# Performance work log

Measured on AMD Instinct MI355X. Metric: run time of the kernel, lower is better.

Reference implementation:

```python
import jax, jax.numpy as jnp
import numpy as np

EPS = 1e-3  # keras BatchNormalization default epsilon


def _bn(x, gamma, beta, mean, var):
    # inference-mode batch norm over last axis
    return gamma * (x - mean) * jax.lax.rsqrt(var + EPS) + beta


def _maxpool_w2(x):
    # MaxPooling2D(pool_size=[1,2], strides=[1,2]) over width axis of NHWC
    B, H, W, C = x.shape
    return x.reshape(B, H, W // 2, 2, C).max(axis=3)


def setup_inputs() -> dict:
    key = jax.random.key(0)
    ks = jax.random.split(key, 12)
    B, H, W, C, Ci = 8, 64, 64, 256, 128
    s = lambda k, shape, scale=0.05: jax.random.normal(k, shape, dtype=jnp.float32) * scale
    return {
        "inputs": jax.random.normal(ks[0], (B, H, W, C), dtype=jnp.float32),
        "bn1_gamma": jnp.ones((C,), jnp.float32), "bn1_beta": jnp.zeros((C,), jnp.float32),
        "bn1_mean": s(ks[1], (C,), 0.1), "bn1_var": jnp.abs(s(ks[2], (C,), 0.1)) + 1.0,
        "bn2_gamma": jnp.ones((Ci,), jnp.float32), "bn2_beta": jnp.zeros((Ci,), jnp.float32),
        "bn2_mean": s(ks[3], (Ci,), 0.1), "bn2_var": jnp.abs(s(ks[4], (Ci,), 0.1)) + 1.0,
        "W_g": s(ks[5], (C, Ci)), "b_g": jnp.zeros((Ci,), jnp.float32),
        "W_theta": s(ks[6], (C, Ci)), "b_theta": jnp.zeros((Ci,), jnp.float32),
        "W_phi": s(ks[7], (C, Ci)), "b_phi": jnp.zeros((Ci,), jnp.float32),
        "W_z": s(ks[8], (Ci, C)), "b_z": jnp.zeros((C,), jnp.float32),
        "sita": s(ks[9], (1,), 0.5),
    }


def reference(inputs, bn1_gamma, bn1_beta, bn1_mean, bn1_var,
              bn2_gamma, bn2_beta, bn2_mean, bn2_var,
              W_g, b_g, W_theta, b_theta, W_phi, b_phi, W_z, b_z, sita):
    B, H, W, C = inputs.shape
    Ci = W_g.shape[1]
    x = jax.nn.elu(_bn(inputs, bn1_gamma, bn1_beta, bn1_mean, bn1_var))
    # 1x1 convs == per-pixel channel matmuls (NHWC)
    g_x = _maxpool_w2(jnp.einsum('bhwc,cd->bhwd', x, W_g) + b_g)          # [B,H,W/2,Ci]
    g_x = g_x.reshape(B, H * (W // 2), Ci)                                  # [B,Ns,Ci]
    theta_x = (jnp.einsum('bhwc,cd->bhwd', x, W_theta) + b_theta).reshape(B, H * W, Ci)  # [B,N,Ci]
    phi_x = _maxpool_w2(jnp.einsum('bhwc,cd->bhwd', x, W_phi) + b_phi)    # [B,H,W/2,Ci]
    phi_x = phi_x.transpose(0, 3, 1, 2).reshape(B, Ci, H * (W // 2))        # [B,Ci,Ns]
    f = jnp.einsum('bnc,bcm->bnm', theta_x, phi_x)                          # [B,N,Ns]
    y = jax.nn.softmax(f, axis=-1)
    y = jnp.einsum('bnm,bmc->bnc', y, g_x).reshape(B, H, W, Ci)
    fre_z = jax.nn.elu(_bn(y, bn2_gamma, bn2_beta, bn2_mean, bn2_var))
    fre_z = jnp.einsum('bhwc,cd->bhwd', fre_z, W_z) + b_z                   # [B,H,W,C]
    return fre_z * sita + inputs
```

## Files before the change

kernel.cpp:

```cpp
#include <hip/hip_runtime.h>
#include <math.h>

#define BNEPS 1e-3f
#define LOG2E 1.44269504f

typedef __attribute__((ext_vector_type(8))) short bf8;
typedef __attribute__((ext_vector_type(8))) unsigned short u16x8;
typedef __attribute__((ext_vector_type(16))) float f32x16;
typedef __attribute__((ext_vector_type(2))) unsigned u32x2;

__device__ __forceinline__ unsigned short f2bf(float x) {
  unsigned u = __builtin_bit_cast(unsigned, x);
  unsigned r = (u + 0x7fffu + ((u >> 16) & 1u)) >> 16;
  return (unsigned short)r;
}
__device__ __forceinline__ float bf2f(unsigned short h) {
  return __builtin_bit_cast(float, ((unsigned)h) << 16);
}
__device__ __forceinline__ float eluf(float v) { return v > 0.f ? v : expm1f(v); }
__device__ __forceinline__ unsigned cvtpk(float a, float b) {
  unsigned r;
  asm("v_cvt_pk_bf16_f32 %0, %1, %2" : "=v"(r) : "v"(a), "v"(b));
  return r;
}
__device__ __forceinline__ float exp2a(float x) {
  float r;
  asm("v_exp_f32 %0, %1" : "=v"(r) : "v"(x));
  return r;
}

#define GLDS(src, dst)                                                          \
  __builtin_amdgcn_global_load_lds(                                             \
      (const __attribute__((address_space(1))) unsigned int*)(src),             \
      (__attribute__((address_space(3))) unsigned int*)(dst), 16, 0, 0)

__global__ __launch_bounds__(256) void k_prepw(
    const float* __restrict__ Wth, const float* __restrict__ Wg,
    const float* __restrict__ Wph, const float* __restrict__ Wz,
    const float* __restrict__ g1, const float* __restrict__ b1,
    const float* __restrict__ m1, const float* __restrict__ v1,
    const float* __restrict__ g2, const float* __restrict__ b2,
    const float* __restrict__ m2, const float* __restrict__ v2,
    unsigned short* __restrict__ Wt3, unsigned short* __restrict__ Wzt,
    float* __restrict__ bn1s, float* __restrict__ bn1h,
    float* __restrict__ bn2s, float* __restrict__ bn2h)
{
  int id = blockIdx.x * 256 + threadIdx.x;
  if (id < 98304) {
    int w = id >> 15, rem = id & 32767;
    int n = rem >> 8, k = rem & 255;
    const float* W = (w == 0) ? Wth : (w == 1) ? Wg : Wph;
    Wt3[id] = f2bf(W[(size_t)k * 128 + n]);
  } else {
    int rem = id - 98304;
    int n = rem >> 7, k = rem & 127;
    Wzt[rem] = f2bf(Wz[(size_t)k * 256 + n]);
  }
  if (id < 256) { float s = g1[id] * rsqrtf(v1[id] + BNEPS); bn1s[id] = s; bn1h[id] = b1[id] - m1[id] * s; }
  if (id < 128) { float s = g2[id] * rsqrtf(v2[id] + BNEPS); bn2s[id] = s; bn2h[id] = b2[id] - m2[id] * s; }
}

__global__ __launch_bounds__(256) void k_gemm3(
    const float* __restrict__ inp, const float* __restrict__ bn1s,
    const float* __restrict__ bn1h, const unsigned short* __restrict__ Wt3,
    const float* __restrict__ bth, const float* __restrict__ bg,
    const float* __restrict__ bph, unsigned short* __restrict__ Tb,
    unsigned short* __restrict__ Gt2, unsigned short* __restrict__ Pp2)
{
  __shared__ unsigned short As[128][72];
  __shared__ unsigned short Bs[128][72];
  const int bm = blockIdx.x * 128;
  const int sel = blockIdx.y;
  const unsigned short* W = Wt3 + (size_t)sel * 32768;
  const float* bias = (sel == 0) ? bth : (sel == 1) ? bg : bph;
  const int tid = threadIdx.x;
  const int l = tid & 63, w = tid >> 6;
  const int lo = l & 31, g = l >> 5;
  const int row = tid >> 1, hf = tid & 1;
  f32x16 acc[4];
#pragma unroll
  for (int i = 0; i < 4; ++i)
#pragma unroll
    for (int j = 0; j < 16; ++j) acc[i][j] = 0.f;

  for (int k0 = 0; k0 < 256; k0 += 64) {
    __syncthreads();
    {
      const float* sa = inp + (size_t)(bm + row) * 256 + k0 + hf * 32;
      unsigned short tmp[32];
#pragma unroll
      for (int i = 0; i < 8; ++i) {
        float4 v = *(const float4*)(sa + i * 4);
        int ch = k0 + hf * 32 + i * 4;
        tmp[i * 4 + 0] = f2bf(eluf(v.x * bn1s[ch + 0] + bn1h[ch + 0]));
        tmp[i * 4 + 1] = f2bf(eluf(v.y * bn1s[ch + 1] + bn1h[ch + 1]));
        tmp[i * 4 + 2] = f2bf(eluf(v.z * bn1s[ch + 2] + bn1h[ch + 2]));
        tmp[i * 4 + 3] = f2bf(eluf(v.w * bn1s[ch + 3] + bn1h[ch + 3]));
      }
#pragma unroll
      for (int i = 0; i < 4; ++i)
        *(u16x8*)&As[row][hf * 32 + i * 8] = *(u16x8*)&tmp[i * 8];
      const unsigned short* sb = W + (size_t)row * 256 + k0 + hf * 32;
#pragma unroll
      for (int i = 0; i < 4; ++i)
        *(u16x8*)&Bs[row][hf * 32 + i * 8] = *(const u16x8*)(sb + i * 8);
    }
    __syncthreads();
#pragma unroll
    for (int ks = 0; ks < 4; ++ks) {
      bf8 af = *(const bf8*)&As[w * 32 + lo][ks * 16 + g * 8];
#pragma unroll
      for (int n2 = 0; n2 < 4; ++n2) {
        bf8 bF = *(const bf8*)&Bs[n2 * 32 + lo][ks * 16 + g * 8];
        acc[n2] = __builtin_amdgcn_mfma_f32_32x32x16_bf16(af, bF, acc[n2], 0, 0, 0);
      }
    }
  }

  if (sel == 0) {
#pragma unroll
    for (int n2 = 0; n2 < 4; ++n2) {
      int col = n2 * 32 + lo;
      float bv = bias[col];
#pragma unroll
      for (int q = 0; q < 4; ++q)
#pragma unroll
        for (int j = 0; j < 4; ++j) {
          size_t r = (size_t)(bm + w * 32 + j + q * 8 + g * 4);
          Tb[r * 128 + col] = f2bf((acc[n2][q * 4 + j] + bv) * LOG2E);
        }
    }
  } else {
#pragma unroll
    for (int n2 = 0; n2 < 4; ++n2) {
      int col = n2 * 32 + lo;
      float bv = bias[col];
#pragma unroll
      for (int q = 0; q < 4; ++q)
#pragma unroll
        for (int jp = 0; jp < 2; ++jp) {
          int j = jp * 2;
          float v0 = acc[n2][q * 4 + j] + bv;
          float v1 = acc[n2][q * 4 + j + 1] + bv;
          float mx = fmaxf(v0, v1);
          int r = bm + w * 32 + q * 8 + g * 4 + j;
          int pr = r >> 1;
          int b = pr >> 11, local = pr & 2047;
          int kb = local >> 5, sub = (local >> 3) & 3, m = local & 7, kv5 = local & 31;
          if (sel == 1)
            Gt2[((((size_t)b * 64 + kb) * 4 + sub) * 128 + col) * 8 + m] = f2bf(mx);
          else
            Pp2[((((size_t)b * 64 + kb) * 16 + (col >> 3)) * 32 + kv5) * 8 + (col & 7)] = f2bf(mx);
        }
    }
  }
}

__global__ __launch_bounds__(128, 4) void k_attn(
    const unsigned short* __restrict__ T, const unsigned short* __restrict__ Pp2,
    const unsigned short* __restrict__ Gt2, unsigned short* __restrict__ Opart,
    float* __restrict__ lpart)
{
  __shared__ unsigned short phl[4096];
  __shared__ unsigned short vtl[4096];
  const int bid = blockIdx.x;
  const int b = bid & 7, qt = (bid >> 3) & 63, sp = bid >> 9;
  const int tid = threadIdx.x;
  const int w = tid >> 6, l = tid & 63;
  const int lo = l & 31, g = l >> 5;
  const int qr0 = qt * 64;

  const unsigned short* Tq = T + ((size_t)(b * 4096 + qr0 + w * 32 + lo)) * 128 + g * 8;
  bf8 qf[8];
#pragma unroll
  for (int ks = 0; ks < 8; ++ks) qf[ks] = *(const bf8*)(Tq + ks * 16);

  f32x16 oacc[4];
#pragma unroll
  for (int i = 0; i < 4; ++i)
#pragma unroll
    for (int j = 0; j < 16; ++j) oacc[i][j] = 0.f;
  float lrun = 0.f;

  const unsigned short* Pc = Pp2 + ((size_t)b * 64 + sp * 16) * 4096;
  const unsigned short* Gc = Gt2 + ((size_t)b * 64 + sp * 16) * 4096;

  for (int it = 0; it < 16; ++it) {
    const unsigned short* ps = Pc + (size_t)it * 4096 + w * 2048 + l * 8;
    const unsigned short* vs = Gc + (size_t)it * 4096 + w * 2048 + l * 8;
#pragma unroll
    for (int j = 0; j < 4; ++j) {
      GLDS(ps + j * 512, &phl[(w * 4 + j) * 512]);
      GLDS(vs + j * 512, &vtl[(w * 4 + j) * 512]);
    }
    __syncthreads();

    f32x16 s0;
#pragma unroll
    for (int j = 0; j < 16; ++j) s0[j] = 0.f;
#pragma unroll
    for (int ks = 0; ks < 8; ++ks) {
      bf8 a0 = *(const bf8*)&phl[(ks * 2 + g) * 256 + lo * 8];
      s0 = __builtin_amdgcn_mfma_f32_32x32x16_bf16(a0, qf[ks], s0, 0, 0, 0);
    }

#pragma unroll
    for (int r = 0; r < 16; ++r) { s0[r] = exp2a(s0[r]); lrun += s0[r]; }

#pragma unroll
    for (int ks2 = 0; ks2 < 2; ++ks2) {
      const int base = 8 * ks2;
      unsigned uA0 = cvtpk(s0[base + 0], s0[base + 1]);
      unsigned uA1 = cvtpk(s0[base + 2], s0[base + 3]);
      unsigned uB0 = cvtpk(s0[base + 4], s0[base + 5]);
      unsigned uB1 = cvtpk(s0[base + 6], s0[base + 7]);
      unsigned sw0 = g ? uA0 : uB0;
      unsigned sw1 = g ? uA1 : uB1;
      unsigned a0 = sw0, b0 = sw0, a1 = sw1, b1 = sw1;
      asm("v_permlane32_swap_b32 %0, %1" : "+v"(a0), "+v"(b0));
      asm("v_permlane32_swap_b32 %0, %1" : "+v"(a1), "+v"(b1));
      unsigned r0 = g ? a0 : b0;
      unsigned r1 = g ? a1 : b1;
      union { bf8 v; unsigned u[4]; } pf;
      if (g == 0) { pf.u[0] = uA0; pf.u[1] = uA1; pf.u[2] = r0; pf.u[3] = r1; }
      else        { pf.u[0] = r0;  pf.u[1] = r1;  pf.u[2] = uB0; pf.u[3] = uB1; }
#pragma unroll
      for (int n2 = 0; n2 < 4; ++n2) {
        bf8 vf = *(const bf8*)&vtl[(ks2 * 2 + g) * 1024 + (n2 * 32 + lo) * 8];
        oacc[n2] = __builtin_amdgcn_mfma_f32_32x32x16_bf16(vf, pf.v, oacc[n2], 0, 0, 0);
      }
    }
    __syncthreads();
  }

  lrun += __shfl_xor(lrun, 32);
  const int qrow = qr0 + w * 32 + lo;
  unsigned short* Ob = Opart + (size_t)sp * 4194304 + ((size_t)(b * 4096 + qrow)) * 128;
#pragma unroll
  for (int n2 = 0; n2 < 4; ++n2)
#pragma unroll
    for (int q4 = 0; q4 < 4; ++q4) {
      unsigned u0 = cvtpk(oacc[n2][q4 * 4 + 0], oacc[n2][q4 * 4 + 1]);
      unsigned u1 = cvtpk(oacc[n2][q4 * 4 + 2], oacc[n2][q4 * 4 + 3]);
      u32x2 o = {u0, u1};
      *(u32x2*)&Ob[n2 * 32 + q4 * 8 + g * 4] = o;
    }
  if (g == 0) lpart[(size_t)sp * 32768 + b * 4096 + qrow] = lrun;
}

__global__ __launch_bounds__(256) void k_gemm_z(
    const unsigned short* __restrict__ Opart, const float* __restrict__ lp,
    const unsigned short* __restrict__ Wzt,
    const float* __restrict__ bz, const float* __restrict__ bn2s,
    const float* __restrict__ bn2h, const float* __restrict__ inp,
    const float* __restrict__ sita, float* __restrict__ out)
{
  __shared__ unsigned short As[128][72];
  __shared__ unsigned short Bs[128][72];
  const int bm = blockIdx.x * 128, n0 = blockIdx.y * 128;
  const int tid = threadIdx.x;
  const int l = tid & 63, w = tid >> 6, lo = l & 31, g = l >> 5;
  const int row = tid >> 1, hf = tid & 1;
  const size_t grow = (size_t)(bm + row);
  const float inv = 1.f / (lp[grow] + lp[32768 + grow] + lp[65536 + grow] + lp[98304 + grow]);
  f32x16 acc[4];
#pragma unroll
  for (int i = 0; i < 4; ++i)
#pragma unroll
    for (int j = 0; j < 16; ++j) acc[i][j] = 0.f;

  for (int k0 = 0; k0 < 128; k0 += 64) {
    __syncthreads();
    {
      unsigned short tmp[32];
#pragma unroll
      for (int i = 0; i < 4; ++i) {
        size_t off = grow * 128 + k0 + hf * 32 + i * 8;
        u16x8 p0 = *(const u16x8*)&Opart[off];
        u16x8 p1 = *(const u16x8*)&Opart[4194304 + off];
        u16x8 p2 = *(const u16x8*)&Opart[8388608 + off];
        u16x8 p3 = *(const u16x8*)&Opart[12582912 + off];
#pragma unroll
        for (int j = 0; j < 8; ++j) {
          int ch = k0 + hf * 32 + i * 8 + j;
          float y = (bf2f(p0[j]) + bf2f(p1[j]) + bf2f(p2[j]) + bf2f(p3[j])) * inv;
          tmp[i * 8 + j] = f2bf(eluf(y * bn2s[ch] + bn2h[ch]));
        }
      }
#pragma unroll
      for (int i = 0; i < 4; ++i)
        *(u16x8*)&As[row][hf * 32 + i * 8] = *(u16x8*)&tmp[i * 8];
      const unsigned short* sb = Wzt + (size_t)(n0 + row) * 128 + k0 + hf * 32;
#pragma unroll
      for (int i = 0; i < 4; ++i)
        *(u16x8*)&Bs[row][hf * 32 + i * 8] = *(const u16x8*)(sb + i * 8);
    }
    __syncthreads();
#pragma unroll
    for (int ks = 0; ks < 4; ++ks) {
      bf8 af = *(const bf8*)&As[w * 32 + lo][ks * 16 + g * 8];
#pragma unroll
      for (int n2 = 0; n2 < 4; ++n2) {
        bf8 bF = *(const bf8*)&Bs[n2 * 32 + lo][ks * 16 + g * 8];
        acc[n2] = __builtin_amdgcn_mfma_f32_32x32x16_bf16(af, bF, acc[n2], 0, 0, 0);
      }
    }
  }
  float st = sita[0];
#pragma unroll
  for (int n2 = 0; n2 < 4; ++n2) {
    int col = n0 + n2 * 32 + lo;
    float bv = bz[col];
#pragma unroll
    for (int q = 0; q < 4; ++q)
#pragma unroll
      for (int j = 0; j < 4; ++j) {
        size_t r = (size_t)(bm + w * 32 + j + q * 8 + g * 4);
        out[r * 256 + col] = (acc[n2][q * 4 + j] + bv) * st + inp[r * 256 + col];
      }
  }
}

extern "C" void kernel_launch(void* const* d_in, const int* in_sizes, int n_in,
                              void* d_out, int out_size, void* d_ws, size_t ws_size,
                              hipStream_t stream) {
  const float* inp   = (const float*)d_in[0];
  const float* bn1_g = (const float*)d_in[1];
  const float* bn1_b = (const float*)d_in[2];
  const float* bn1_m = (const float*)d_in[3];
  const float* bn1_v = (const float*)d_in[4];
  const float* bn2_g = (const float*)d_in[5];
  const float* bn2_b = (const float*)d_in[6];
  const float* bn2_m = (const float*)d_in[7];
  const float* bn2_v = (const float*)d_in[8];
  const float* W_g   = (const float*)d_in[9];
  const float* b_g   = (const float*)d_in[10];
  const float* W_th  = (const float*)d_in[11];
  const float* b_th  = (const float*)d_in[12];
  const float* W_ph  = (const float*)d_in[13];
  const float* b_ph  = (const float*)d_in[14];
  const float* W_z   = (const float*)d_in[15];
  const float* b_z   = (const float*)d_in[16];
  const float* sita  = (const float*)d_in[17];
  float* out = (float*)d_out;

  float* ws_f = (float*)d_ws;
  float* lp   = ws_f;
  float* bn1s = lp + 131072;
  float* bn1h = bn1s + 256;
  float* bn2s = bn1h + 256;
  float* bn2h = bn2s + 128;
  unsigned short* Opart = (unsigned short*)(bn2h + 128);
  unsigned short* Tb  = Opart + 16777216;
  unsigned short* Gt2 = Tb + 4194304;
  unsigned short* Pp2 = Gt2 + 2097152;
  unsigned short* Wt3 = Pp2 + 2097152;
  unsigned short* Wzt = Wt3 + 98304;

  k_prepw<<<dim3(512), dim3(256), 0, stream>>>(W_th, W_g, W_ph, W_z,
                                               bn1_g, bn1_b, bn1_m, bn1_v,
                                               bn2_g, bn2_b, bn2_m, bn2_v,
                                               Wt3, Wzt, bn1s, bn1h, bn2s, bn2h);
  k_gemm3<<<dim3(256, 3), dim3(256), 0, stream>>>(inp, bn1s, bn1h, Wt3,
                                                  b_th, b_g, b_ph, Tb, Gt2, Pp2);
  k_attn<<<dim3(2048), dim3(128), 0, stream>>>(Tb, Pp2, Gt2, Opart, lp);
  k_gemm_z<<<dim3(256, 2), dim3(256), 0, stream>>>(Opart, lp, Wzt, b_z,
                                                   bn2s, bn2h, inp, sita, out);
}
```

Baseline: 251.3 us.

## Fuse three projection GEMMs into one pass with fragment-packed weights

```diff
diff --git a/kernel.cpp b/kernel.cpp
--- a/kernel.cpp
+++ b/kernel.cpp
@@ -17,15 +17,17 @@
 __device__ __forceinline__ float bf2f(unsigned short h) {
   return __builtin_bit_cast(float, ((unsigned)h) << 16);
 }
-__device__ __forceinline__ float eluf(float v) { return v > 0.f ? v : expm1f(v); }
+__device__ __forceinline__ float exp2a(float x) {
+  float r;
+  asm("v_exp_f32 %0, %1" : "=v"(r) : "v"(x));
+  return r;
+}
+__device__ __forceinline__ float eluf(float v) {
+  return v > 0.f ? v : exp2a(v * LOG2E) - 1.f;
+}
 __device__ __forceinline__ unsigned cvtpk(float a, float b) {
   unsigned r;
   asm("v_cvt_pk_bf16_f32 %0, %1, %2" : "=v"(r) : "v"(a), "v"(b));
-  return r;
-}
-__device__ __forceinline__ float exp2a(float x) {
-  float r;
-  asm("v_exp_f32 %0, %1" : "=v"(r) : "v"(x));
   return r;
 }
 
@@ -41,16 +43,21 @@
     const float* __restrict__ m1, const float* __restrict__ v1,
     const float* __restrict__ g2, const float* __restrict__ b2,
     const float* __restrict__ m2, const float* __restrict__ v2,
-    unsigned short* __restrict__ Wt3, unsigned short* __restrict__ Wzt,
+    unsigned short* __restrict__ Wfrag, unsigned short* __restrict__ Wzt,
     float* __restrict__ bn1s, float* __restrict__ bn1h,
     float* __restrict__ bn2s, float* __restrict__ bn2h)
 {
   int id = blockIdx.x * 256 + threadIdx.x;
   if (id < 98304) {
-    int w = id >> 15, rem = id & 32767;
-    int n = rem >> 8, k = rem & 255;
-    const float* W = (w == 0) ? Wth : (w == 1) ? Wg : Wph;
-    Wt3[id] = f2bf(W[(size_t)k * 128 + n]);
+    int e = id & 7, lo = (id >> 3) & 31;
+    int fg = id >> 8;
+    int f = fg % 12;
+    int r = fg / 12;
+    int g = r & 1, ks = (r >> 1) & 3, t = r >> 3;
+    int sel = f >> 2, n2 = f & 3;
+    int n = n2 * 32 + lo, k = t * 64 + ks * 16 + g * 8 + e;
+    const float* W = (sel == 0) ? Wth : (sel == 1) ? Wg : Wph;
+    Wfrag[id] = f2bf(W[(size_t)k * 128 + n]);
   } else {
     int rem = id - 98304;
     int n = rem >> 7, k = rem & 127;
@@ -60,98 +67,115 @@
   if (id < 128) { float s = g2[id] * rsqrtf(v2[id] + BNEPS); bn2s[id] = s; bn2h[id] = b2[id] - m2[id] * s; }
 }
 
-__global__ __launch_bounds__(256) void k_gemm3(
+__global__ __launch_bounds__(256, 2) void k_gemm3(
     const float* __restrict__ inp, const float* __restrict__ bn1s,
-    const float* __restrict__ bn1h, const unsigned short* __restrict__ Wt3,
+    const float* __restrict__ bn1h, const unsigned short* __restrict__ Wfrag,
     const float* __restrict__ bth, const float* __restrict__ bg,
     const float* __restrict__ bph, unsigned short* __restrict__ Tb,
     unsigned short* __restrict__ Gt2, unsigned short* __restrict__ Pp2)
 {
-  __shared__ unsigned short As[128][72];
-  __shared__ unsigned short Bs[128][72];
-  const int bm = blockIdx.x * 128;
-  const int sel = blockIdx.y;
-  const unsigned short* W = Wt3 + (size_t)sel * 32768;
-  const float* bias = (sel == 0) ? bth : (sel == 1) ? bg : bph;
+  __shared__ unsigned short As[64][72];
+  __shared__ unsigned short Tt[64][136];
+  __shared__ float2 bnsh[256];
+  const int bm = blockIdx.x * 64;
   const int tid = threadIdx.x;
-  const int l = tid & 63, w = tid >> 6;
+  const int w = tid >> 6, l = tid & 63;
   const int lo = l & 31, g = l >> 5;
-  const int row = tid >> 1, hf = tid & 1;
-  f32x16 acc[4];
-#pragma unroll
-  for (int i = 0; i < 4; ++i)
+  const int wm = w & 1, nb = (w >> 1) * 6;
+  const int srow = tid >> 2, sq = tid & 3;
+  if (tid < 256) bnsh[tid] = {bn1s[tid], bn1h[tid]};
+
+  f32x16 acc[6];
+#pragma unroll
+  for (int i = 0; i < 6; ++i)
 #pragma unroll
     for (int j = 0; j < 16; ++j) acc[i][j] = 0.f;
 
-  for (int k0 = 0; k0 < 256; k0 += 64) {
+  for (int t = 0; t < 4; ++t) {
     __syncthreads();
     {
-      const float* sa = inp + (size_t)(bm + row) * 256 + k0 + hf * 32;
-      unsigned short tmp[32];
-#pragma unroll
-      for (int i = 0; i < 8; ++i) {
-        float4 v = *(const float4*)(sa + i * 4);
-        int ch = k0 + hf * 32 + i * 4;
-        tmp[i * 4 + 0] = f2bf(eluf(v.x * bn1s[ch + 0] + bn1h[ch + 0]));
-        tmp[i * 4 + 1] = f2bf(eluf(v.y * bn1s[ch + 1] + bn1h[ch + 1]));
-        tmp[i * 4 + 2] = f2bf(eluf(v.z * bn1s[ch + 2] + bn1h[ch + 2]));
-        tmp[i * 4 + 3] = f2bf(eluf(v.w * bn1s[ch + 3] + bn1h[ch + 3]));
-      }
-#pragma unroll
-      for (int i = 0; i < 4; ++i)
-        *(u16x8*)&As[row][hf * 32 + i * 8] = *(u16x8*)&tmp[i * 8];
-      const unsigned short* sb = W + (size_t)row * 256 + k0 + hf * 32;
-#pragma unroll
-      for (int i = 0; i < 4; ++i)
-        *(u16x8*)&Bs[row][hf * 32 + i * 8] = *(const u16x8*)(sb + i * 8);
+      const float* sa = inp + (size_t)(bm + srow) * 256 + t * 64 + sq * 16;
+#pragma unroll
+      for (int h = 0; h < 2; ++h) {
+        float4 v0 = *(const float4*)(sa + h * 8);
+        float4 v1 = *(const float4*)(sa + h * 8 + 4);
+        int ch = t * 64 + sq * 16 + h * 8;
+        float vv[8] = {v0.x, v0.y, v0.z, v0.w, v1.x, v1.y, v1.z, v1.w};
+        u16x8 o;
+#pragma unroll
+        for (int u = 0; u < 8; ++u) {
+          float2 sh = bnsh[ch + u];
+          o[u] = f2bf(eluf(vv[u] * sh.x + sh.y));
+        }
+        *(u16x8*)&As[srow][sq * 16 + h * 8] = o;
+      }
     }
     __syncthreads();
 #pragma unroll
     for (int ks = 0; ks < 4; ++ks) {
-      bf8 af = *(const bf8*)&As[w * 32 + lo][ks * 16 + g * 8];
-#pragma unroll
-      for (int n2 = 0; n2 < 4; ++n2) {
-        bf8 bF = *(const bf8*)&Bs[n2 * 32 + lo][ks * 16 + g * 8];
-        acc[n2] = __builtin_amdgcn_mfma_f32_32x32x16_bf16(af, bF, acc[n2], 0, 0, 0);
-      }
-    }
-  }
-
-  if (sel == 0) {
-#pragma unroll
-    for (int n2 = 0; n2 < 4; ++n2) {
-      int col = n2 * 32 + lo;
-      float bv = bias[col];
+      bf8 af = *(const bf8*)&As[wm * 32 + lo][ks * 16 + g * 8];
+      const unsigned short* wf =
+          Wfrag + (size_t)((((t * 4 + ks) * 2 + g) * 12 + nb) * 32 + lo) * 8;
+#pragma unroll
+      for (int fi = 0; fi < 6; ++fi) {
+        bf8 bF = *(const bf8*)(wf + fi * 256);
+        acc[fi] = __builtin_amdgcn_mfma_f32_32x32x16_bf16(af, bF, acc[fi], 0, 0, 0);
+      }
+    }
+  }
+
+#pragma unroll
+  for (int fi = 0; fi < 6; ++fi) {
+    const int fg = nb + fi;
+    if (fg < 4) {
+      int col = fg * 32 + lo;
+      float bv = bth[col];
 #pragma unroll
       for (int q = 0; q < 4; ++q)
 #pragma unroll
-        for (int j = 0; j < 4; ++j) {
-          size_t r = (size_t)(bm + w * 32 + j + q * 8 + g * 4);
-          Tb[r * 128 + col] = f2bf((acc[n2][q * 4 + j] + bv) * LOG2E);
-        }
-    }
-  } else {
-#pragma unroll
-    for (int n2 = 0; n2 < 4; ++n2) {
-      int col = n2 * 32 + lo;
-      float bv = bias[col];
-#pragma unroll
-      for (int q = 0; q < 4; ++q)
-#pragma unroll
-        for (int jp = 0; jp < 2; ++jp) {
-          int j = jp * 2;
-          float v0 = acc[n2][q * 4 + j] + bv;
-          float v1 = acc[n2][q * 4 + j + 1] + bv;
-          float mx = fmaxf(v0, v1);
-          int r = bm + w * 32 + q * 8 + g * 4 + j;
-          int pr = r >> 1;
-          int b = pr >> 11, local = pr & 2047;
-          int kb = local >> 5, sub = (local >> 3) & 3, m = local & 7, kv5 = local & 31;
-          if (sel == 1)
-            Gt2[((((size_t)b * 64 + kb) * 4 + sub) * 128 + col) * 8 + m] = f2bf(mx);
-          else
-            Pp2[((((size_t)b * 64 + kb) * 16 + (col >> 3)) * 32 + kv5) * 8 + (col & 7)] = f2bf(mx);
-        }
+        for (int j = 0; j < 4; ++j)
+          Tt[wm * 32 + q * 8 + g * 4 + j][col] = f2bf((acc[fi][q * 4 + j] + bv) * LOG2E);
+    } else if (fg < 8) {
+      int col = (fg - 4) * 32 + lo;
+      float bv = bg[col];
+#pragma unroll
+      for (int q = 0; q < 4; ++q) {
+        float v0 = acc[fi][q * 4 + 0] + bv, v1 = acc[fi][q * 4 + 1] + bv;
+        float v2 = acc[fi][q * 4 + 2] + bv, v3 = acc[fi][q * 4 + 3] + bv;
+        float mx01 = fmaxf(v0, v1), mx23 = fmaxf(v2, v3);
+        int r = bm + wm * 32 + q * 8 + g * 4;
+        int pr = r >> 1;
+        int b = pr >> 11, local = pr & 2047;
+        int kb = local >> 5, sub = (local >> 3) & 3, m = local & 7;
+        unsigned pk = cvtpk(mx01, mx23);
+        *(unsigned*)&Gt2[((((size_t)b * 64 + kb) * 4 + sub) * 128 + col) * 8 + m] = pk;
+      }
+    } else {
+      int col = (fg - 8) * 32 + lo;
+      float bv = bph[col];
+      int csub = col >> 3, e = col & 7;
+#pragma unroll
+      for (int q = 0; q < 4; ++q) {
+        float v0 = acc[fi][q * 4 + 0] + bv, v1 = acc[fi][q * 4 + 1] + bv;
+        float v2 = acc[fi][q * 4 + 2] + bv, v3 = acc[fi][q * 4 + 3] + bv;
+        float mx01 = fmaxf(v0, v1), mx23 = fmaxf(v2, v3);
+        int r = bm + wm * 32 + q * 8 + g * 4;
+        int pr = r >> 1;
+        int b = pr >> 11, local = pr & 2047;
+        int kb = local >> 5, kv = local & 31;
+        size_t base = (((size_t)(b * 64 + kb) * 16 + csub) * 32 + kv) * 8 + e;
+        Pp2[base] = f2bf(mx01);
+        Pp2[base + 8] = f2bf(mx23);
+      }
+    }
+  }
+  __syncthreads();
+  {
+    const int rr = tid >> 2, qq = tid & 3;
+#pragma unroll
+    for (int i = 0; i < 4; ++i) {
+      u16x8 vv = *(u16x8*)&Tt[rr][qq * 32 + i * 8];
+      *(u16x8*)&Tb[(size_t)(bm + rr) * 128 + qq * 32 + i * 8] = vv;
     }
   }
 }
@@ -195,6 +219,7 @@
     }
     __syncthreads();
 
+    __builtin_amdgcn_s_setprio(1);
     f32x16 s0;
 #pragma unroll
     for (int j = 0; j < 16; ++j) s0[j] = 0.f;
@@ -203,10 +228,12 @@
       bf8 a0 = *(const bf8*)&phl[(ks * 2 + g) * 256 + lo * 8];
       s0 = __builtin_amdgcn_mfma_f32_32x32x16_bf16(a0, qf[ks], s0, 0, 0, 0);
     }
+    __builtin_amdgcn_s_setprio(0);
 
 #pragma unroll
     for (int r = 0; r < 16; ++r) { s0[r] = exp2a(s0[r]); lrun += s0[r]; }
 
+    __builtin_amdgcn_s_setprio(1);
 #pragma unroll
     for (int ks2 = 0; ks2 < 2; ++ks2) {
       const int base = 8 * ks2;
@@ -230,6 +257,7 @@
         oacc[n2] = __builtin_amdgcn_mfma_f32_32x32x16_bf16(vf, pf.v, oacc[n2], 0, 0, 0);
       }
     }
+    __builtin_amdgcn_s_setprio(0);
     __syncthreads();
   }
 
@@ -354,15 +382,15 @@
   unsigned short* Tb  = Opart + 16777216;
   unsigned short* Gt2 = Tb + 4194304;
   unsigned short* Pp2 = Gt2 + 2097152;
-  unsigned short* Wt3 = Pp2 + 2097152;
-  unsigned short* Wzt = Wt3 + 98304;
+  unsigned short* Wfr = Pp2 + 2097152;
+  unsigned short* Wzt = Wfr + 98304;
 
   k_prepw<<<dim3(512), dim3(256), 0, stream>>>(W_th, W_g, W_ph, W_z,
                                                bn1_g, bn1_b, bn1_m, bn1_v,
                                                bn2_g, bn2_b, bn2_m, bn2_v,
-                                               Wt3, Wzt, bn1s, bn1h, bn2s, bn2h);
-  k_gemm3<<<dim3(256, 3), dim3(256), 0, stream>>>(inp, bn1s, bn1h, Wt3,
-                                                  b_th, b_g, b_ph, Tb, Gt2, Pp2);
+                                               Wfr, Wzt, bn1s, bn1h, bn2s, bn2h);
+  k_gemm3<<<dim3(512), dim3(256), 0, stream>>>(inp, bn1s, bn1h, Wfr,
+                                               b_th, b_g, b_ph, Tb, Gt2, Pp2);
   k_attn<<<dim3(2048), dim3(128), 0, stream>>>(Tb, Pp2, Gt2, Opart, lp);
   k_gemm_z<<<dim3(256, 2), dim3(256), 0, stream>>>(Opart, lp, Wzt, b_z,
                                                    bn2s, bn2h, inp, sita, out);
```

Measured after the change: 222.8 us. 1.13x faster.
